# Kernel tuning notes

Hardware: AMD Instinct MI355X
Metric: run time of the kernel (lower is better)

The kernel has to match this reference:

```python
import jax, jax.numpy as jnp
import numpy as np

NUM_HEADS = 16
THETA = 10000.0


def apply_rope(x, positions, theta=THETA):
    # x: [B, H, S, d_k], positions: [B, S] (broadcast over heads)
    d_k = x.shape[-1]
    inv_freq = theta ** (-jnp.arange(0, d_k // 2, dtype=jnp.float32) * 2.0 / d_k)  # [d_k/2]
    ang = positions[:, None, :, None].astype(jnp.float32) * inv_freq  # [B,1,S,d_k/2]
    cos, sin = jnp.cos(ang), jnp.sin(ang)
    x1 = x[..., 0::2]
    x2 = x[..., 1::2]
    r1 = x1 * cos - x2 * sin
    r2 = x1 * sin + x2 * cos
    # interleave back: [..., d_k/2, 2] -> [..., d_k]
    return jnp.stack([r1, r2], axis=-1).reshape(x.shape)


def setup_inputs() -> dict:
    key = jax.random.key(0)
    ks = jax.random.split(key, 5)
    B, S, D = 1, 4096, 1024
    scale = 1.0 / np.sqrt(D)
    x = jax.random.normal(ks[0], (B, S, D), dtype=jnp.float32)
    Wq = jax.random.normal(ks[1], (D, D), dtype=jnp.float32) * scale
    Wk = jax.random.normal(ks[2], (D, D), dtype=jnp.float32) * scale
    Wv = jax.random.normal(ks[3], (D, D), dtype=jnp.float32) * scale
    Wo = jax.random.normal(ks[4], (D, D), dtype=jnp.float32) * scale
    token_positions = jnp.broadcast_to(jnp.arange(S, dtype=jnp.int32), (B, S))
    return {"x": x, "token_positions": token_positions, "Wq": Wq, "Wk": Wk, "Wv": Wv, "Wo": Wo}


def reference(x, token_positions, Wq, Wk, Wv, Wo):
    B, S, D = x.shape
    H = NUM_HEADS
    d_k = D // H
    # fused QKV projection (Linear: y = x @ W^T, no bias)
    q = jnp.einsum('bsd,ed->bse', x, Wq)
    k = jnp.einsum('bsd,ed->bse', x, Wk)
    v = jnp.einsum('bsd,ed->bse', x, Wv)
    # [B,S,H*dk] -> [B,H,S,dk]
    Q = q.reshape(B, S, H, d_k).transpose(0, 2, 1, 3)
    K = k.reshape(B, S, H, d_k).transpose(0, 2, 1, 3)
    V = v.reshape(B, S, H, d_k).transpose(0, 2, 1, 3)
    Q = apply_rope(Q, token_positions)
    K = apply_rope(K, token_positions)
    scores = jnp.einsum('bhqd,bhkd->bhqk', Q, K) / jnp.sqrt(jnp.float32(d_k))
    causal = jnp.tril(jnp.ones((S, S), dtype=bool))
    scores = jnp.where(causal, scores, -jnp.inf)
    P = jax.nn.softmax(scores, axis=-1)
    out = jnp.einsum('bhqk,bhkd->bhqd', P, V)  # [B,H,S,dk]
    out = out.transpose(0, 2, 1, 3).reshape(B, S, D)
    return jnp.einsum('bsd,ed->bse', out, Wo)
```

## Files before the change

### kernel.cpp

```cpp
#include <hip/hip_runtime.h>
#include <hip/hip_bf16.h>
#include <stdint.h>

#define S_LEN   4096
#define D_MODEL 1024
#define NHEAD   16
#define DK      64

typedef __attribute__((ext_vector_type(8))) __bf16 bf16x8;
typedef __attribute__((ext_vector_type(4))) float  f32x4;
using bf16 = __hip_bfloat16;

__device__ __forceinline__ void load_lds16(const bf16* g, bf16* l) {
    __builtin_amdgcn_global_load_lds(
        (const __attribute__((address_space(1))) void*)g,
        (__attribute__((address_space(3))) void*)l, 16, 0, 0);
}

__global__ void cvt_all(const float* __restrict__ x,
                        const float* __restrict__ w0, const float* __restrict__ w1,
                        const float* __restrict__ w2, const float* __restrict__ w3,
                        bf16* __restrict__ xb,
                        bf16* __restrict__ b0, bf16* __restrict__ b1,
                        bf16* __restrict__ b2, bf16* __restrict__ b3)
{
    size_t i4 = ((size_t)blockIdx.x * 256 + threadIdx.x) * 4;
    const float* s; bf16* d; size_t off;
    const size_t NX = (size_t)S_LEN * D_MODEL;
    const size_t NW = (size_t)D_MODEL * D_MODEL;
    if (i4 < NX) { s = x; d = xb; off = i4; }
    else {
        size_t j = i4 - NX;
        int sel = (int)(j >> 20);
        off = j & (NW - 1);
        s = sel == 0 ? w0 : sel == 1 ? w1 : sel == 2 ? w2 : w3;
        d = sel == 0 ? b0 : sel == 1 ? b1 : sel == 2 ? b2 : b3;
    }
    float4 v = *(const float4*)&s[off];
    bf16 t[4] __attribute__((aligned(8)));
    t[0] = __float2bfloat16(v.x); t[1] = __float2bfloat16(v.y);
    t[2] = __float2bfloat16(v.z); t[3] = __float2bfloat16(v.w);
    *(uint64_t*)&d[off] = *(const uint64_t*)t;
}

__global__ __launch_bounds__(256) void qkv_gemm(
    const bf16* __restrict__ Xb,
    const bf16* __restrict__ Wq, const bf16* __restrict__ Wk, const bf16* __restrict__ Wv,
    float* __restrict__ Qf, float* __restrict__ Kf, bf16* __restrict__ VtG)
{
    const int K = D_MODEL, N = D_MODEL;
    int z = blockIdx.z;
    const bf16* B = (z == 0) ? Wq : (z == 1) ? Wk : Wv;

    __shared__ __align__(16) bf16 As[2][128 * 32];
    __shared__ __align__(16) bf16 Bs[2][128 * 32];
    __shared__ __align__(16) bf16 Ts[4][64 * 24];

    int row0 = blockIdx.y * 128;
    int col0 = blockIdx.x * 128;
    int tid  = threadIdx.x;
    int wv   = tid >> 6, lane = tid & 63;
    int m16  = lane & 15, quad = lane >> 4;
    int wr   = (wv >> 1) * 64, wc = (wv & 1) * 64;
    int l4   = lane >> 2, l3 = (lane & 3) * 8;

    const bf16* ga_base = Xb + (size_t)(row0 + wv * 16 + l4) * K + l3;
    const bf16* gb_base = B  + (size_t)(col0 + wv * 16 + l4) * K + l3;

    auto stage = [&](int k0, int buf) {
        load_lds16(ga_base + k0,            &As[buf][wv * 512]);
        load_lds16(ga_base + k0 + 64 * K,   &As[buf][2048 + wv * 512]);
        load_lds16(gb_base + k0,            &Bs[buf][wv * 512]);
        load_lds16(gb_base + k0 + 64 * K,   &Bs[buf][2048 + wv * 512]);
    };

    f32x4 acc[4][4];
    #pragma unroll
    for (int i = 0; i < 4; i++)
        #pragma unroll
        for (int j = 0; j < 4; j++) acc[i][j] = (f32x4){0.f, 0.f, 0.f, 0.f};

    stage(0, 0);
    for (int k0 = 0; k0 < K; k0 += 32) {
        __syncthreads();
        int buf = (k0 >> 5) & 1;
        if (k0 + 32 < K) stage(k0 + 32, buf ^ 1);
        bf16x8 a[4], b[4];
        #pragma unroll
        for (int mi = 0; mi < 4; mi++) a[mi] = *(const bf16x8*)&As[buf][(wr + mi * 16 + m16) * 32 + quad * 8];
        #pragma unroll
        for (int ni = 0; ni < 4; ni++) b[ni] = *(const bf16x8*)&Bs[buf][(wc + ni * 16 + m16) * 32 + quad * 8];
        #pragma unroll
        for (int mi = 0; mi < 4; mi++)
            #pragma unroll
            for (int ni = 0; ni < 4; ni++)
                acc[mi][ni] = __builtin_amdgcn_mfma_f32_16x16x32_bf16(a[mi], b[ni], acc[mi][ni], 0, 0, 0);
    }

    if (z < 2) {
        float* O = (z == 0) ? Qf : Kf;
        #pragma unroll
        for (int mi = 0; mi < 4; mi++)
            #pragma unroll
            for (int ni = 0; ni < 4; ni++)
                #pragma unroll
                for (int r = 0; r < 4; r++) {
                    int gr = row0 + wr + mi * 16 + quad * 4 + r;
                    int gc = col0 + wc + ni * 16 + m16;
                    O[(size_t)gr * N + gc] = acc[mi][ni][r];
                }
    } else {
        #pragma unroll
        for (int mi = 0; mi < 4; mi++) {
            #pragma unroll
            for (int nt = 0; nt < 4; nt++) {
                bf16 t4[4] __attribute__((aligned(8)));
                #pragma unroll
                for (int r = 0; r < 4; r++) t4[r] = __float2bfloat16(acc[mi][nt][r]);
                *(uint64_t*)&Ts[wv][(nt * 16 + m16) * 24 + quad * 4] = *(const uint64_t*)t4;
            }
            #pragma unroll
            for (int rep = 0; rep < 2; rep++) {
                int c  = (lane >> 1) + rep * 32;
                int r8 = lane & 1;
                bf16x8 val = *(const bf16x8*)&Ts[wv][c * 24 + r8 * 8];
                int gc = col0 + wc + c;
                int gr = row0 + wr + mi * 16 + r8 * 8;
                *(bf16x8*)&VtG[(size_t)gc * S_LEN + gr] = val;
            }
        }
    }
}

__global__ __launch_bounds__(256) void out_gemm(
    const bf16* __restrict__ A_, const bf16* __restrict__ B,
    float* __restrict__ C)
{
    const int K = D_MODEL, N = D_MODEL;
    __shared__ __align__(16) bf16 As[2][128 * 32];
    __shared__ __align__(16) bf16 Bs[2][128 * 32];

    int row0 = blockIdx.y * 128;
    int col0 = blockIdx.x * 128;
    int tid  = threadIdx.x;
    int wv   = tid >> 6, lane = tid & 63;
    int m16  = lane & 15, quad = lane >> 4;
    int wr   = (wv >> 1) * 64, wc = (wv & 1) * 64;
    int l4   = lane >> 2, l3 = (lane & 3) * 8;

    const bf16* ga_base = A_ + (size_t)(row0 + wv * 16 + l4) * K + l3;
    const bf16* gb_base = B  + (size_t)(col0 + wv * 16 + l4) * K + l3;

    auto stage = [&](int k0, int buf) {
        load_lds16(ga_base + k0,            &As[buf][wv * 512]);
        load_lds16(ga_base + k0 + 64 * K,   &As[buf][2048 + wv * 512]);
        load_lds16(gb_base + k0,            &Bs[buf][wv * 512]);
        load_lds16(gb_base + k0 + 64 * K,   &Bs[buf][2048 + wv * 512]);
    };

    f32x4 acc[4][4];
    #pragma unroll
    for (int i = 0; i < 4; i++)
        #pragma unroll
        for (int j = 0; j < 4; j++) acc[i][j] = (f32x4){0.f, 0.f, 0.f, 0.f};

    stage(0, 0);
    for (int k0 = 0; k0 < K; k0 += 32) {
        __syncthreads();
        int buf = (k0 >> 5) & 1;
        if (k0 + 32 < K) stage(k0 + 32, buf ^ 1);
        bf16x8 a[4], b[4];
        #pragma unroll
        for (int mi = 0; mi < 4; mi++) a[mi] = *(const bf16x8*)&As[buf][(wr + mi * 16 + m16) * 32 + quad * 8];
        #pragma unroll
        for (int ni = 0; ni < 4; ni++) b[ni] = *(const bf16x8*)&Bs[buf][(wc + ni * 16 + m16) * 32 + quad * 8];
        #pragma unroll
        for (int mi = 0; mi < 4; mi++)
            #pragma unroll
            for (int ni = 0; ni < 4; ni++)
                acc[mi][ni] = __builtin_amdgcn_mfma_f32_16x16x32_bf16(a[mi], b[ni], acc[mi][ni], 0, 0, 0);
    }

    #pragma unroll
    for (int mi = 0; mi < 4; mi++)
        #pragma unroll
        for (int ni = 0; ni < 4; ni++)
            #pragma unroll
            for (int r = 0; r < 4; r++) {
                int gr = row0 + wr + mi * 16 + quad * 4 + r;
                int gc = col0 + wc + ni * 16 + m16;
                C[(size_t)gr * N + gc] = acc[mi][ni][r];
            }
}

__global__ void rope_kernel(const float* __restrict__ Qf, const float* __restrict__ Kf,
                            const int* __restrict__ pos,
                            bf16* __restrict__ Qb, bf16* __restrict__ Kb)
{
    int gid = blockIdx.x * 256 + threadIdx.x;
    size_t i8 = (size_t)gid * 8;
    int s   = (int)(i8 >> 10);
    int col = (int)(i8 & 1023);
    int pair0 = (col & 63) >> 1;
    float p = (float)pos[s];

    float4 qa = *(const float4*)&Qf[i8];
    float4 qb_ = *(const float4*)&Qf[i8 + 4];
    float4 ka = *(const float4*)&Kf[i8];
    float4 kb_ = *(const float4*)&Kf[i8 + 4];
    float q[8] = {qa.x, qa.y, qa.z, qa.w, qb_.x, qb_.y, qb_.z, qb_.w};
    float k[8] = {ka.x, ka.y, ka.z, ka.w, kb_.x, kb_.y, kb_.z, kb_.w};

    bf16 oq[8] __attribute__((aligned(16)));
    bf16 ok[8] __attribute__((aligned(16)));
    const float scale = 0.125f;
    const float c0 = -0.41524101186092028f;
    #pragma unroll
    for (int j = 0; j < 4; j++) {
        float fi = (float)(pair0 + j);
        float inv = exp2f(fi * (-0.41524101186092028f));
        (void)c0;
        float ang = p * inv;
        float sn, cs;
        __sincosf(ang, &sn, &cs);
        float q1 = q[2 * j], q2 = q[2 * j + 1];
        float k1 = k[2 * j], k2 = k[2 * j + 1];
        oq[2 * j]     = __float2bfloat16((q1 * cs - q2 * sn) * scale);
        oq[2 * j + 1] = __float2bfloat16((q1 * sn + q2 * cs) * scale);
        ok[2 * j]     = __float2bfloat16(k1 * cs - k2 * sn);
        ok[2 * j + 1] = __float2bfloat16(k1 * sn + k2 * cs);
    }
    *(bf16x8*)&Qb[i8] = *(const bf16x8*)oq;
    *(bf16x8*)&Kb[i8] = *(const bf16x8*)ok;
}

__global__ __launch_bounds__(256) void attn_kernel(
    const bf16* __restrict__ Qb, const bf16* __restrict__ Kb, const bf16* __restrict__ VtG,
    bf16* __restrict__ Attn)
{
    int bx  = blockIdx.x;
    int h   = bx & 15;
    int qt  = 63 - (bx >> 4);
    int tid = threadIdx.x;
    int wv  = tid >> 6, lane = tid & 63;
    int m16 = lane & 15, quad = lane >> 4;
    int l4  = lane >> 2, l3 = (lane & 3) * 8;
    int q0  = qt * 64;
    int hc  = h * DK;

    __shared__ __align__(16) bf16 KT[2][2][64 * 32];
    __shared__ __align__(16) bf16 VT[2][2][64 * 32];
    __shared__ __align__(16) bf16 Ps[64 * 72];

    const bf16* kg = Kb  + (size_t)(wv * 16 + l4) * D_MODEL + hc + l3;
    const bf16* vg = VtG + (size_t)(hc + wv * 16 + l4) * S_LEN + l3;

    auto stage = [&](int kb, int buf) {
        size_t ko = (size_t)kb * 64;
        load_lds16(kg + ko * D_MODEL,        &KT[buf][0][wv * 512]);
        load_lds16(kg + ko * D_MODEL + 32,   &KT[buf][1][wv * 512]);
        load_lds16(vg + ko,                  &VT[buf][0][wv * 512]);
        load_lds16(vg + ko + 32,             &VT[buf][1][wv * 512]);
    };

    const int qrow = q0 + wv * 16 + m16;
    bf16x8 aq0 = *(const bf16x8*)&Qb[(size_t)qrow * D_MODEL + hc + quad * 8];
    bf16x8 aq1 = *(const bf16x8*)&Qb[(size_t)qrow * D_MODEL + hc + 32 + quad * 8];

    float l_part[4];
    f32x4 o[4];
    #pragma unroll
    for (int r = 0; r < 4; r++) l_part[r] = 0.f;
    #pragma unroll
    for (int t = 0; t < 4; t++) o[t] = (f32x4){0.f, 0.f, 0.f, 0.f};

    const float SHIFT = 8.0f;

    stage(0, 0);
    for (int kb = 0; kb <= qt; ++kb) {
        __syncthreads();
        int buf = kb & 1;
        if (kb < qt) stage(kb + 1, buf ^ 1);
        int kbase = kb * 64;

        f32x4 sAcc[4];
        #pragma unroll
        for (int nt = 0; nt < 4; nt++) {
            bf16x8 b0 = *(const bf16x8*)&KT[buf][0][(nt * 16 + m16) * 32 + quad * 8];
            bf16x8 b1 = *(const bf16x8*)&KT[buf][1][(nt * 16 + m16) * 32 + quad * 8];
            f32x4 zv = (f32x4){0.f, 0.f, 0.f, 0.f};
            zv = __builtin_amdgcn_mfma_f32_16x16x32_bf16(aq0, b0, zv, 0, 0, 0);
            zv = __builtin_amdgcn_mfma_f32_16x16x32_bf16(aq1, b1, zv, 0, 0, 0);
            sAcc[nt] = zv;
        }

        if (kb == qt) {
            #pragma unroll
            for (int nt = 0; nt < 4; nt++) {
                int colg = kbase + nt * 16 + m16;
                #pragma unroll
                for (int r = 0; r < 4; r++) {
                    int rowg = q0 + wv * 16 + quad * 4 + r;
                    if (colg > rowg) sAcc[nt][r] = -1e30f;
                }
            }
        }

        #pragma unroll
        for (int nt = 0; nt < 4; nt++) {
            #pragma unroll
            for (int r = 0; r < 4; r++) {
                float pv = __expf(sAcc[nt][r] - SHIFT);
                sAcc[nt][r] = pv;
                l_part[r] += pv;
            }
        }

        #pragma unroll
        for (int nt = 0; nt < 4; nt++)
            #pragma unroll
            for (int r = 0; r < 4; r++)
                Ps[(wv * 16 + quad * 4 + r) * 72 + nt * 16 + m16] = __float2bfloat16(sAcc[nt][r]);

        bf16x8 ap0 = *(const bf16x8*)&Ps[(wv * 16 + m16) * 72 + quad * 8];
        bf16x8 ap1 = *(const bf16x8*)&Ps[(wv * 16 + m16) * 72 + 32 + quad * 8];

        #pragma unroll
        for (int nt = 0; nt < 4; nt++) {
            bf16x8 b0 = *(const bf16x8*)&VT[buf][0][(nt * 16 + m16) * 32 + quad * 8];
            bf16x8 b1 = *(const bf16x8*)&VT[buf][1][(nt * 16 + m16) * 32 + quad * 8];
            o[nt] = __builtin_amdgcn_mfma_f32_16x16x32_bf16(ap0, b0, o[nt], 0, 0, 0);
            o[nt] = __builtin_amdgcn_mfma_f32_16x16x32_bf16(ap1, b1, o[nt], 0, 0, 0);
        }
    }

    float inv[4];
    #pragma unroll
    for (int r = 0; r < 4; r++) {
        float l = l_part[r];
        l += __shfl_xor(l, 1); l += __shfl_xor(l, 2);
        l += __shfl_xor(l, 4); l += __shfl_xor(l, 8);
        inv[r] = 1.0f / l;
    }
    #pragma unroll
    for (int nt = 0; nt < 4; nt++)
        #pragma unroll
        for (int r = 0; r < 4; r++) {
            int rowg = q0 + wv * 16 + quad * 4 + r;
            Attn[(size_t)rowg * D_MODEL + hc + nt * 16 + m16] = __float2bfloat16(o[nt][r] * inv[r]);
        }
}

extern "C" void kernel_launch(void* const* d_in, const int* in_sizes, int n_in,
                              void* d_out, int out_size, void* d_ws, size_t ws_size,
                              hipStream_t stream)
{
    const float* x  = (const float*)d_in[0];
    const int*   pos= (const int*)d_in[1];
    const float* Wq = (const float*)d_in[2];
    const float* Wk = (const float*)d_in[3];
    const float* Wv = (const float*)d_in[4];
    const float* Wo = (const float*)d_in[5];
    float* out = (float*)d_out;

    char* ws = (char*)d_ws;
    bf16*  xb   = (bf16*) (ws);
    bf16*  wqb  = (bf16*) (ws + ( 8ull << 20));
    bf16*  wkb  = (bf16*) (ws + (10ull << 20));
    bf16*  wvb  = (bf16*) (ws + (12ull << 20));
    bf16*  wob  = (bf16*) (ws + (14ull << 20));
    float* Qf   = (float*)(ws + (16ull << 20));
    float* Kf   = (float*)(ws + (32ull << 20));
    bf16*  Qb   = (bf16*) (ws + (48ull << 20));
    bf16*  Kb   = (bf16*) (ws + (56ull << 20));
    bf16*  VtG  = (bf16*) (ws + (64ull << 20));
    bf16*  Attn = (bf16*) (ws + (72ull << 20));

    cvt_all<<<8192, 256, 0, stream>>>(x, Wq, Wk, Wv, Wo, xb, wqb, wkb, wvb, wob);

    qkv_gemm<<<dim3(8, 32, 3), 256, 0, stream>>>(xb, wqb, wkb, wvb, Qf, Kf, VtG);

    rope_kernel<<<2048, 256, 0, stream>>>(Qf, Kf, pos, Qb, Kb);

    attn_kernel<<<dim3(1024), 256, 0, stream>>>(Qb, Kb, VtG, Attn);

    out_gemm<<<dim3(8, 32), 256, 0, stream>>>(Attn, wob, out);
}
```

Baseline: 222.2 us.

## Fuse RoPE into QKV epilogue, load K/V directly in attention, shrink out-GEMM tiles

RoPE and the Q scaling, with log2e folded in, move into the QKV GEMM epilogue, using a lane shuffle to pair adjacent columns. This removes the fp32 Q/K round-trip and the separate rope kernel. The attention kernel drops the LDS double-buffered K/V staging and has each lane load its MFMA operands straight from global memory. Softmax switches to exp2. The output GEMM uses 64-row tiles to double the grid size. Direct global loads lose the async prefetch overlap and may raise latency exposure. The smaller out-GEMM tiles reduce operand reuse.

```diff
diff --git a/kernel.cpp b/kernel.cpp
--- a/kernel.cpp
+++ b/kernel.cpp
@@ -10,6 +10,9 @@
 typedef __attribute__((ext_vector_type(8))) __bf16 bf16x8;
 typedef __attribute__((ext_vector_type(4))) float  f32x4;
 using bf16 = __hip_bfloat16;
+
+#define LOG2E     1.44269504f
+#define FREQ_C    0.41524101186092028f
 
 __device__ __forceinline__ void load_lds16(const bf16* g, bf16* l) {
     __builtin_amdgcn_global_load_lds(
@@ -46,7 +49,8 @@
 __global__ __launch_bounds__(256) void qkv_gemm(
     const bf16* __restrict__ Xb,
     const bf16* __restrict__ Wq, const bf16* __restrict__ Wk, const bf16* __restrict__ Wv,
-    float* __restrict__ Qf, float* __restrict__ Kf, bf16* __restrict__ VtG)
+    const int* __restrict__ pos,
+    bf16* __restrict__ Qb, bf16* __restrict__ Kb, bf16* __restrict__ VtG)
 {
     const int K = D_MODEL, N = D_MODEL;
     int z = blockIdx.z;
@@ -98,17 +102,33 @@
     }
 
     if (z < 2) {
-        float* O = (z == 0) ? Qf : Kf;
-        #pragma unroll
-        for (int mi = 0; mi < 4; mi++)
-            #pragma unroll
-            for (int ni = 0; ni < 4; ni++)
+        bf16* O = (z == 0) ? Qb : Kb;
+        const float qscale = (z == 0) ? 0.125f * LOG2E : 1.0f;
+        const bool odd = (m16 & 1);
+        float invf[4];
+        #pragma unroll
+        for (int ni = 0; ni < 4; ni++) {
+            int hd = (wc + ni * 16 + m16) & 63;
+            invf[ni] = exp2f(-(float)(hd >> 1) * FREQ_C);
+        }
+        #pragma unroll
+        for (int mi = 0; mi < 4; mi++) {
+            #pragma unroll
+            for (int r = 0; r < 4; r++) {
+                int gr = row0 + wr + mi * 16 + quad * 4 + r;
+                float p = (float)pos[gr];
                 #pragma unroll
-                for (int r = 0; r < 4; r++) {
-                    int gr = row0 + wr + mi * 16 + quad * 4 + r;
+                for (int ni = 0; ni < 4; ni++) {
+                    float own = acc[mi][ni][r];
+                    float other = __shfl_xor(own, 1);
+                    float sn, cs;
+                    __sincosf(p * invf[ni], &sn, &cs);
+                    float rot = odd ? (other * sn + own * cs) : (own * cs - other * sn);
                     int gc = col0 + wc + ni * 16 + m16;
-                    O[(size_t)gr * N + gc] = acc[mi][ni][r];
+                    O[(size_t)gr * N + gc] = __float2bfloat16(rot * qscale);
                 }
+            }
+        }
     } else {
         #pragma unroll
         for (int mi = 0; mi < 4; mi++) {
@@ -137,15 +157,15 @@
     float* __restrict__ C)
 {
     const int K = D_MODEL, N = D_MODEL;
-    __shared__ __align__(16) bf16 As[2][128 * 32];
+    __shared__ __align__(16) bf16 As[2][64 * 32];
     __shared__ __align__(16) bf16 Bs[2][128 * 32];
 
-    int row0 = blockIdx.y * 128;
+    int row0 = blockIdx.y * 64;
     int col0 = blockIdx.x * 128;
     int tid  = threadIdx.x;
     int wv   = tid >> 6, lane = tid & 63;
     int m16  = lane & 15, quad = lane >> 4;
-    int wr   = (wv >> 1) * 64, wc = (wv & 1) * 64;
+    int wr   = (wv >> 1) * 32, wc = (wv & 1) * 64;
     int l4   = lane >> 2, l3 = (lane & 3) * 8;
 
     const bf16* ga_base = A_ + (size_t)(row0 + wv * 16 + l4) * K + l3;
@@ -153,14 +173,13 @@
 
     auto stage = [&](int k0, int buf) {
         load_lds16(ga_base + k0,            &As[buf][wv * 512]);
-        load_lds16(ga_base + k0 + 64 * K,   &As[buf][2048 + wv * 512]);
         load_lds16(gb_base + k0,            &Bs[buf][wv * 512]);
         load_lds16(gb_base + k0 + 64 * K,   &Bs[buf][2048 + wv * 512]);
     };
 
-    f32x4 acc[4][4];
-    #pragma unroll
-    for (int i = 0; i < 4; i++)
+    f32x4 acc[2][4];
+    #pragma unroll
+    for (int i = 0; i < 2; i++)
         #pragma unroll
         for (int j = 0; j < 4; j++) acc[i][j] = (f32x4){0.f, 0.f, 0.f, 0.f};
 
@@ -169,20 +188,20 @@
         __syncthreads();
         int buf = (k0 >> 5) & 1;
         if (k0 + 32 < K) stage(k0 + 32, buf ^ 1);
-        bf16x8 a[4], b[4];
-        #pragma unroll
-        for (int mi = 0; mi < 4; mi++) a[mi] = *(const bf16x8*)&As[buf][(wr + mi * 16 + m16) * 32 + quad * 8];
+        bf16x8 a[2], b[4];
+        #pragma unroll
+        for (int mi = 0; mi < 2; mi++) a[mi] = *(const bf16x8*)&As[buf][(wr + mi * 16 + m16) * 32 + quad * 8];
         #pragma unroll
         for (int ni = 0; ni < 4; ni++) b[ni] = *(const bf16x8*)&Bs[buf][(wc + ni * 16 + m16) * 32 + quad * 8];
         #pragma unroll
-        for (int mi = 0; mi < 4; mi++)
+        for (int mi = 0; mi < 2; mi++)
             #pragma unroll
             for (int ni = 0; ni < 4; ni++)
                 acc[mi][ni] = __builtin_amdgcn_mfma_f32_16x16x32_bf16(a[mi], b[ni], acc[mi][ni], 0, 0, 0);
     }
 
     #pragma unroll
-    for (int mi = 0; mi < 4; mi++)
+    for (int mi = 0; mi < 2; mi++)
         #pragma unroll
         for (int ni = 0; ni < 4; ni++)
             #pragma unroll
@@ -191,47 +210,6 @@
                 int gc = col0 + wc + ni * 16 + m16;
                 C[(size_t)gr * N + gc] = acc[mi][ni][r];
             }
-}
-
-__global__ void rope_kernel(const float* __restrict__ Qf, const float* __restrict__ Kf,
-                            const int* __restrict__ pos,
-                            bf16* __restrict__ Qb, bf16* __restrict__ Kb)
-{
-    int gid = blockIdx.x * 256 + threadIdx.x;
-    size_t i8 = (size_t)gid * 8;
-    int s   = (int)(i8 >> 10);
-    int col = (int)(i8 & 1023);
-    int pair0 = (col & 63) >> 1;
-    float p = (float)pos[s];
-
-    float4 qa = *(const float4*)&Qf[i8];
-    float4 qb_ = *(const float4*)&Qf[i8 + 4];
-    float4 ka = *(const float4*)&Kf[i8];
-    float4 kb_ = *(const float4*)&Kf[i8 + 4];
-    float q[8] = {qa.x, qa.y, qa.z, qa.w, qb_.x, qb_.y, qb_.z, qb_.w};
-    float k[8] = {ka.x, ka.y, ka.z, ka.w, kb_.x, kb_.y, kb_.z, kb_.w};
-
-    bf16 oq[8] __attribute__((aligned(16)));
-    bf16 ok[8] __attribute__((aligned(16)));
-    const float scale = 0.125f;
-    const float c0 = -0.41524101186092028f;
-    #pragma unroll
-    for (int j = 0; j < 4; j++) {
-        float fi = (float)(pair0 + j);
-        float inv = exp2f(fi * (-0.41524101186092028f));
-        (void)c0;
-        float ang = p * inv;
-        float sn, cs;
-        __sincosf(ang, &sn, &cs);
-        float q1 = q[2 * j], q2 = q[2 * j + 1];
-        float k1 = k[2 * j], k2 = k[2 * j + 1];
-        oq[2 * j]     = __float2bfloat16((q1 * cs - q2 * sn) * scale);
-        oq[2 * j + 1] = __float2bfloat16((q1 * sn + q2 * cs) * scale);
-        ok[2 * j]     = __float2bfloat16(k1 * cs - k2 * sn);
-        ok[2 * j + 1] = __float2bfloat16(k1 * sn + k2 * cs);
-    }
-    *(bf16x8*)&Qb[i8] = *(const bf16x8*)oq;
-    *(bf16x8*)&Kb[i8] = *(const bf16x8*)ok;
 }
 
 __global__ __launch_bounds__(256) void attn_kernel(
@@ -244,24 +222,18 @@
     int tid = threadIdx.x;
     int wv  = tid >> 6, lane = tid & 63;
     int m16 = lane & 15, quad = lane >> 4;
-    int l4  = lane >> 2, l3 = (lane & 3) * 8;
     int q0  = qt * 64;
     int hc  = h * DK;
 
-    __shared__ __align__(16) bf16 KT[2][2][64 * 32];
-    __shared__ __align__(16) bf16 VT[2][2][64 * 32];
     __shared__ __align__(16) bf16 Ps[64 * 72];
 
-    const bf16* kg = Kb  + (size_t)(wv * 16 + l4) * D_MODEL + hc + l3;
-    const bf16* vg = VtG + (size_t)(hc + wv * 16 + l4) * S_LEN + l3;
-
-    auto stage = [&](int kb, int buf) {
-        size_t ko = (size_t)kb * 64;
-        load_lds16(kg + ko * D_MODEL,        &KT[buf][0][wv * 512]);
-        load_lds16(kg + ko * D_MODEL + 32,   &KT[buf][1][wv * 512]);
-        load_lds16(vg + ko,                  &VT[buf][0][wv * 512]);
-        load_lds16(vg + ko + 32,             &VT[buf][1][wv * 512]);
-    };
+    const bf16* kp[4];
+    const bf16* vp[4];
+    #pragma unroll
+    for (int nt = 0; nt < 4; nt++) {
+        kp[nt] = Kb  + (size_t)(nt * 16 + m16) * D_MODEL + hc + quad * 8;
+        vp[nt] = VtG + (size_t)(hc + nt * 16 + m16) * S_LEN + quad * 8;
+    }
 
     const int qrow = q0 + wv * 16 + m16;
     bf16x8 aq0 = *(const bf16x8*)&Qb[(size_t)qrow * D_MODEL + hc + quad * 8];
@@ -274,23 +246,27 @@
     #pragma unroll
     for (int t = 0; t < 4; t++) o[t] = (f32x4){0.f, 0.f, 0.f, 0.f};
 
-    const float SHIFT = 8.0f;
-
-    stage(0, 0);
+    const float SHIFT2 = 8.0f * LOG2E;
+
     for (int kb = 0; kb <= qt; ++kb) {
-        __syncthreads();
-        int buf = kb & 1;
-        if (kb < qt) stage(kb + 1, buf ^ 1);
         int kbase = kb * 64;
+        size_t koD = (size_t)kbase * D_MODEL;
+
+        bf16x8 k0[4], k1[4], v0[4], v1[4];
+        #pragma unroll
+        for (int nt = 0; nt < 4; nt++) {
+            k0[nt] = *(const bf16x8*)(kp[nt] + koD);
+            k1[nt] = *(const bf16x8*)(kp[nt] + koD + 32);
+            v0[nt] = *(const bf16x8*)(vp[nt] + kbase);
+            v1[nt] = *(const bf16x8*)(vp[nt] + kbase + 32);
+        }
 
         f32x4 sAcc[4];
         #pragma unroll
         for (int nt = 0; nt < 4; nt++) {
-            bf16x8 b0 = *(const bf16x8*)&KT[buf][0][(nt * 16 + m16) * 32 + quad * 8];
-            bf16x8 b1 = *(const bf16x8*)&KT[buf][1][(nt * 16 + m16) * 32 + quad * 8];
             f32x4 zv = (f32x4){0.f, 0.f, 0.f, 0.f};
-            zv = __builtin_amdgcn_mfma_f32_16x16x32_bf16(aq0, b0, zv, 0, 0, 0);
-            zv = __builtin_amdgcn_mfma_f32_16x16x32_bf16(aq1, b1, zv, 0, 0, 0);
+            zv = __builtin_amdgcn_mfma_f32_16x16x32_bf16(aq0, k0[nt], zv, 0, 0, 0);
+            zv = __builtin_amdgcn_mfma_f32_16x16x32_bf16(aq1, k1[nt], zv, 0, 0, 0);
             sAcc[nt] = zv;
         }
 
@@ -310,7 +286,7 @@
         for (int nt = 0; nt < 4; nt++) {
             #pragma unroll
             for (int r = 0; r < 4; r++) {
-                float pv = __expf(sAcc[nt][r] - SHIFT);
+                float pv = exp2f(sAcc[nt][r] - SHIFT2);
                 sAcc[nt][r] = pv;
                 l_part[r] += pv;
             }
@@ -327,10 +303,8 @@
 
         #pragma unroll
         for (int nt = 0; nt < 4; nt++) {
-            bf16x8 b0 = *(const bf16x8*)&VT[buf][0][(nt * 16 + m16) * 32 + quad * 8];
-            bf16x8 b1 = *(const bf16x8*)&VT[buf][1][(nt * 16 + m16) * 32 + quad * 8];
-            o[nt] = __builtin_amdgcn_mfma_f32_16x16x32_bf16(ap0, b0, o[nt], 0, 0, 0);
-            o[nt] = __builtin_amdgcn_mfma_f32_16x16x32_bf16(ap1, b1, o[nt], 0, 0, 0);
+            o[nt] = __builtin_amdgcn_mfma_f32_16x16x32_bf16(ap0, v0[nt], o[nt], 0, 0, 0);
+            o[nt] = __builtin_amdgcn_mfma_f32_16x16x32_bf16(ap1, v1[nt], o[nt], 0, 0, 0);
         }
     }
 
@@ -369,20 +343,16 @@
     bf16*  wkb  = (bf16*) (ws + (10ull << 20));
     bf16*  wvb  = (bf16*) (ws + (12ull << 20));
     bf16*  wob  = (bf16*) (ws + (14ull << 20));
-    float* Qf   = (float*)(ws + (16ull << 20));
-    float* Kf   = (float*)(ws + (32ull << 20));
-    bf16*  Qb   = (bf16*) (ws + (48ull << 20));
-    bf16*  Kb   = (bf16*) (ws + (56ull << 20));
-    bf16*  VtG  = (bf16*) (ws + (64ull << 20));
-    bf16*  Attn = (bf16*) (ws + (72ull << 20));
+    bf16*  Qb   = (bf16*) (ws + (16ull << 20));
+    bf16*  Kb   = (bf16*) (ws + (24ull << 20));
+    bf16*  VtG  = (bf16*) (ws + (32ull << 20));
+    bf16*  Attn = (bf16*) (ws + (40ull << 20));
 
     cvt_all<<<8192, 256, 0, stream>>>(x, Wq, Wk, Wv, Wo, xb, wqb, wkb, wvb, wob);
 
-    qkv_gemm<<<dim3(8, 32, 3), 256, 0, stream>>>(xb, wqb, wkb, wvb, Qf, Kf, VtG);
-
-    rope_kernel<<<2048, 256, 0, stream>>>(Qf, Kf, pos, Qb, Kb);
+    qkv_gemm<<<dim3(8, 32, 3), 256, 0, stream>>>(xb, wqb, wkb, wvb, pos, Qb, Kb, VtG);
 
     attn_kernel<<<dim3(1024), 256, 0, stream>>>(Qb, Kb, VtG, Attn);
 
-    out_gemm<<<dim3(8, 32), 256, 0, stream>>>(Attn, wob, out);
-}
+    out_gemm<<<dim3(8, 64), 256, 0, stream>>>(Attn, wob, out);
+}
```

Result: slower. 399.6 us (+79.8%).
